# Performance work log

Measured on AMD Instinct MI355X. Metric: run time of the kernel, lower is better.

## Reference

```python
import jax, jax.numpy as jnp
import numpy as np

N_NODES = 50000
N_EDGES = 1600000
HIDDEN = 64
HEADS = 8
EPS = 1e-16  # matches PyG segment-softmax denominator epsilon


def setup_inputs() -> dict:
    key = jax.random.key(0)
    ks = jax.random.split(key, 8)
    node_features = jax.random.normal(ks[0], (N_NODES,), dtype=jnp.float32)
    edge_index = jax.random.randint(ks[1], (2, N_EDGES), 0, N_NODES, dtype=jnp.int64)
    cycle_mask = jax.random.uniform(ks[2], (N_EDGES,), dtype=jnp.float32)
    # feature_proj: Linear(1, HIDDEN)
    W_proj = jax.random.normal(ks[3], (HIDDEN, 1), dtype=jnp.float32) * 0.5
    b_proj = jax.random.normal(ks[4], (HIDDEN,), dtype=jnp.float32) * 0.1
    # attention_net: Linear(2*HIDDEN+1, HEADS)
    fan_in = 2 * HIDDEN + 1
    W_att = jax.random.normal(ks[5], (HEADS, fan_in), dtype=jnp.float32) / np.sqrt(fan_in)
    b_att = jax.random.normal(ks[6], (HEADS,), dtype=jnp.float32) * 0.1
    cycle_penalty = jnp.full((HEADS,), -1.0, dtype=jnp.float32)
    min_sum_scaler = jnp.array([0.8], dtype=jnp.float32)
    return {
        "node_features": node_features,
        "cycle_mask": cycle_mask,
        "W_proj": W_proj,
        "b_proj": b_proj,
        "W_att": W_att,
        "b_att": b_att,
        "cycle_penalty": cycle_penalty,
        "min_sum_scaler": min_sum_scaler,
        "edge_index": edge_index,
    }


def reference(node_features, cycle_mask, W_proj, b_proj, W_att, b_att,
              cycle_penalty, min_sum_scaler, edge_index):
    src = edge_index[0]
    dst = edge_index[1]
    n = node_features.shape[0]
    w = W_proj[:, 0]  # [H]
    # per-edge projected features: [E, H]
    x_src = node_features[src][:, None] * w[None, :] + b_proj
    x_dst = node_features[dst][:, None] * w[None, :] + b_proj
    att_input = jnp.concatenate([x_src, x_dst, cycle_mask[:, None]], axis=-1)  # [E, 2H+1]
    raw = att_input @ W_att.T + b_att  # [E, heads]
    raw = jnp.where(raw >= 0, raw, 0.2 * raw)  # leaky_relu(0.2)
    raw = raw + cycle_mask[:, None] * cycle_penalty
    # segment softmax over edges grouped by dst
    seg_max = jax.ops.segment_max(raw, dst, num_segments=n)  # [N, heads]
    e = jnp.exp(raw - seg_max[dst])
    seg_sum = jax.ops.segment_sum(e, dst, num_segments=n)
    attn = e / (seg_sum[dst] + EPS)  # [E, heads]
    mean_attn = attn.mean(axis=-1)  # [E]
    messages = node_features[src] * mean_attn * min_sum_scaler[0]
    out = jax.ops.segment_sum(messages, dst, num_segments=n)
    return out
```

## Files before the change

### kernel.cpp

```cpp
#include <hip/hip_runtime.h>

#define N_NODES 50000
#define N_EDGES 1600000
#define HEADS 8
#define HIDDEN 64
#define FAN_IN (2*HIDDEN + 1)
#define EPSF 1e-16f

#define BBITS 8
#define BSIZE 256
#define NB 196
#define NH 256
#define NT 512
#define EPB 6250
#define SCAN_N (NB * NH)
#define STRIP 49
#define CAP 12032

#define CST_OFF   0
#define CNT_OFF   4096
#define BASE_OFF  262144
#define PAY_OFF   1048576
#define DLOC_OFF  (PAY_OFF + (size_t)N_EDGES * 8)
#define WS_NEEDED (DLOC_OFF + (size_t)N_EDGES)

__global__ __launch_bounds__(512) void k_prep(
    const float* __restrict__ Wp, const float* __restrict__ bp,
    const float* __restrict__ Wa, const float* __restrict__ ba,
    const float* __restrict__ cp, float* __restrict__ cst) {
    const int k = threadIdx.x >> 6;
    const int j = threadIdx.x & 63;
    const float* row = Wa + k * FAN_IN;
    const float w = Wp[j], b = bp[j];
    const float r1 = row[j], r2 = row[HIDDEN + j];
    float a1 = w * r1, a2 = w * r2, d = b * (r1 + r2);
    #pragma unroll
    for (int s = 32; s > 0; s >>= 1) {
        a1 += __shfl_xor(a1, s);
        a2 += __shfl_xor(a2, s);
        d  += __shfl_xor(d, s);
    }
    if (j == 0) {
        cst[k]      = a1;
        cst[8 + k]  = a2;
        cst[16 + k] = row[2 * HIDDEN];
        cst[24 + k] = d + ba[k];
        cst[32 + k] = cp[k];
    }
}

__global__ __launch_bounds__(NT) void k1a_hist(const int* __restrict__ ei,
                                               int* __restrict__ cnt) {
    __shared__ int hist[NB];
    const int t = threadIdx.x, blk = blockIdx.x;
    if (t < NB) hist[t] = 0;
    __syncthreads();
    const int e0 = blk * EPB, e1 = min(e0 + EPB, N_EDGES);
    for (int e = e0 + t; e < e1; e += NT)
        atomicAdd(&hist[((unsigned)ei[N_EDGES + e]) >> BBITS], 1);
    __syncthreads();
    if (t < NB) cnt[t * NH + blk] = hist[t];
}

__global__ __launch_bounds__(1024) void k_scan(const int* __restrict__ cnt,
                                               int* __restrict__ base) {
    __shared__ int lds[1024];
    const int t = threadIdx.x;
    int s = 0;
    #pragma unroll
    for (int jj = 0; jj < STRIP; ++jj) s += cnt[t * STRIP + jj];
    lds[t] = s;
    __syncthreads();
    for (int d = 1; d < 1024; d <<= 1) {
        const int v = (t >= d) ? lds[t - d] : 0;
        __syncthreads();
        lds[t] += v;
        __syncthreads();
    }
    int run = lds[t] - s;
    #pragma unroll
    for (int jj = 0; jj < STRIP; ++jj) {
        const int i = t * STRIP + jj;
        const int v = cnt[i];
        base[i] = run;
        run += v;
    }
}

__global__ __launch_bounds__(NT) void k1b_scatter(const int* __restrict__ ei,
                                                  const float* __restrict__ cmask,
                                                  const float* __restrict__ nf,
                                                  const int* __restrict__ base,
                                                  float2* __restrict__ pay,
                                                  unsigned char* __restrict__ dloc) {
    __shared__ int cur[NB];
    const int t = threadIdx.x, blk = blockIdx.x;
    if (t < NB) cur[t] = base[t * NH + blk];
    __syncthreads();
    const int e0 = blk * EPB, e1 = min(e0 + EPB, N_EDGES);
    for (int e = e0 + t; e < e1; e += NT) {
        const int src = ei[e];
        const int dst = ei[N_EDGES + e];
        const float fs = nf[src];
        const float c  = cmask[e];
        const int bkt = ((unsigned)dst) >> BBITS;
        const int pos = atomicAdd(&cur[bkt], 1);
        pay[pos]  = make_float2(fs, c);
        dloc[pos] = (unsigned char)(dst & (BSIZE - 1));
    }
}

__global__ __launch_bounds__(NT) void k2_fused(const float* __restrict__ nf,
                                               const float* __restrict__ cst_g,
                                               const int* __restrict__ base,
                                               const float2* __restrict__ pay,
                                               const unsigned char* __restrict__ dloc,
                                               const float* __restrict__ scaler,
                                               float* __restrict__ out) {
    __shared__ float2 pbuf[CAP];
    __shared__ int    hist[BSIZE];
    __shared__ int    noff[BSIZE + 1];
    __shared__ float  FD[BSIZE];
    __shared__ float  cstl[40];

    const int t = threadIdx.x, b = blockIdx.x;
    if (t < 40) cstl[t] = cst_g[t];
    if (t < BSIZE) {
        hist[t] = 0;
        const int n = b * BSIZE + t;
        FD[t] = (n < N_NODES) ? nf[n] : 0.f;
    }
    if (t == NT - 1) noff[0] = 0;
    __syncthreads();

    const int i0 = base[b * NH];
    const int i1 = (b == NB - 1) ? N_EDGES : base[(b + 1) * NH];

    for (int i = i0 + t; i < i1; i += NT)
        atomicAdd(&hist[dloc[i]], 1);
    __syncthreads();

    if (t < BSIZE) noff[t + 1] = hist[t];
    __syncthreads();
    for (int d = 1; d < BSIZE; d <<= 1) {
        int v = 0;
        if (t < BSIZE && t >= d) v = noff[t + 1 - d];
        __syncthreads();
        if (t < BSIZE && t >= d) noff[t + 1] += v;
        __syncthreads();
    }
    if (t < BSIZE) hist[t] = noff[t];
    __syncthreads();

    for (int i = i0 + t; i < i1; i += NT) {
        const int dl = dloc[i];
        const int p  = atomicAdd(&hist[dl], 1);
        if (p < CAP) pbuf[p] = pay[i];
    }
    __syncthreads();

    float A1[8], A2[8], CC[8], DD[8], PP[8];
    #pragma unroll
    for (int k = 0; k < 8; ++k) {
        A1[k] = cstl[k];      A2[k] = cstl[8 + k];  CC[k] = cstl[16 + k];
        DD[k] = cstl[24 + k]; PP[k] = cstl[32 + k];
    }

    const int j = t >> 1, par = t & 1;
    const int n = b * BSIZE + j;
    if (n < N_NODES) {
        int lo = noff[j], hi = noff[j + 1];
        lo = min(lo, CAP); hi = min(hi, CAP);
        const float fd = FD[j];
        float as[8], at[8];
        #pragma unroll
        for (int k = 0; k < 8; ++k) { as[k] = 0.f; at[k] = 0.f; }
        for (int i = lo + par; i < hi; i += 2) {
            const float2 p = pbuf[i];
            #pragma unroll
            for (int k = 0; k < 8; ++k) {
                float r = p.x * A1[k] + fd * A2[k] + p.y * CC[k] + DD[k];
                r = (r >= 0.f) ? r : 0.2f * r;
                r += p.y * PP[k];
                const float ev = __expf(r);
                as[k] += ev;
                at[k] += p.x * ev;
            }
        }
        #pragma unroll
        for (int k = 0; k < 8; ++k) {
            as[k] += __shfl_xor(as[k], 1);
            at[k] += __shfl_xor(at[k], 1);
        }
        if (par == 0) {
            float acc = 0.f;
            #pragma unroll
            for (int k = 0; k < 8; ++k) acc += at[k] / (as[k] + EPSF);
            out[n] = acc * 0.125f * scaler[0];
        }
    }
}

__global__ __launch_bounds__(256) void cagat_edge_atomic(
    const float* __restrict__ nf, const float* __restrict__ cmask,
    const float* __restrict__ Wp, const float* __restrict__ bp,
    const float* __restrict__ Wa, const float* __restrict__ ba,
    const float* __restrict__ cp, const int* __restrict__ ei,
    float* __restrict__ S, float* __restrict__ T) {
    __shared__ float A1[HEADS], A2[HEADS], CC[HEADS], DD[HEADS], PP[HEADS];
    const int t = threadIdx.x;
    if (t < HEADS) {
        const float* row = Wa + t * FAN_IN;
        float a1 = 0.f, a2 = 0.f, d = 0.f;
        for (int h = 0; h < HIDDEN; ++h) {
            float w = Wp[h], b = bp[h];
            a1 += w * row[h]; a2 += w * row[HIDDEN + h];
            d += b * (row[h] + row[HIDDEN + h]);
        }
        A1[t] = a1; A2[t] = a2; CC[t] = row[2*HIDDEN]; DD[t] = d + ba[t]; PP[t] = cp[t];
    }
    __syncthreads();
    const int e = blockIdx.x * 256 + t;
    if (e >= N_EDGES) return;
    const int src = ei[e], dst = ei[N_EDGES + e];
    const float fs = nf[src], fd = nf[dst], c = cmask[e];
    #pragma unroll
    for (int k = 0; k < HEADS; ++k) {
        float r = fs * A1[k] + fd * A2[k] + c * CC[k] + DD[k];
        r = (r >= 0.f) ? r : 0.2f * r;
        r += c * PP[k];
        float ev = __expf(r);
        atomicAdd(S + dst * HEADS + k, ev);
        atomicAdd(T + dst * HEADS + k, fs * ev);
    }
}

__global__ __launch_bounds__(256) void cagat_node_atomic(
    const float* __restrict__ S, const float* __restrict__ T,
    const float* __restrict__ scaler, float* __restrict__ out) {
    const int n = blockIdx.x * 256 + threadIdx.x;
    if (n >= N_NODES) return;
    float acc = 0.f;
    #pragma unroll
    for (int k = 0; k < HEADS; ++k)
        acc += T[n * HEADS + k] / (S[n * HEADS + k] + EPSF);
    out[n] = acc * 0.125f * scaler[0];
}

extern "C" void kernel_launch(void* const* d_in, const int* in_sizes, int n_in,
                              void* d_out, int out_size, void* d_ws, size_t ws_size,
                              hipStream_t stream) {
    const float* nf    = (const float*)d_in[0];
    const float* cmask = (const float*)d_in[1];
    const float* Wp    = (const float*)d_in[2];
    const float* bp    = (const float*)d_in[3];
    const float* Wa    = (const float*)d_in[4];
    const float* ba    = (const float*)d_in[5];
    const float* cp    = (const float*)d_in[6];
    const float* sc    = (const float*)d_in[7];
    const int*   ei    = (const int*)d_in[8];

    char* ws = (char*)d_ws;

    if (ws_size >= WS_NEEDED) {
        float*         cst  = (float*)(ws + CST_OFF);
        int*           cnt  = (int*)(ws + CNT_OFF);
        int*           base = (int*)(ws + BASE_OFF);
        float2*        pay  = (float2*)(ws + PAY_OFF);
        unsigned char* dl   = (unsigned char*)(ws + DLOC_OFF);

        k_prep<<<1, 512, 0, stream>>>(Wp, bp, Wa, ba, cp, cst);
        k1a_hist<<<NH, NT, 0, stream>>>(ei, cnt);
        k_scan<<<1, 1024, 0, stream>>>(cnt, base);
        k1b_scatter<<<NH, NT, 0, stream>>>(ei, cmask, nf, base, pay, dl);
        k2_fused<<<NB, NT, 0, stream>>>(nf, cst, base, pay, dl, sc, (float*)d_out);
    } else {
        float* S = (float*)d_ws;
        float* T = S + (size_t)N_NODES * HEADS;
        hipMemsetAsync(d_ws, 0, (size_t)N_NODES * HEADS * 2 * sizeof(float), stream);
        cagat_edge_atomic<<<(N_EDGES + 255) / 256, 256, 0, stream>>>(
            nf, cmask, Wp, bp, Wa, ba, cp, ei, S, T);
        cagat_node_atomic<<<(N_NODES + 255) / 256, 256, 0, stream>>>(
            S, T, sc, (float*)d_out);
    }
}
```

Measured before the change: 155.2 us.

## Fuse bucket-sort pipeline into one cooperative kernel with grid syncs

Replaces the five-kernel pipeline (prep, histogram, scan, scatter, aggregate) with a single cooperative kernel of 256 blocks that uses grid.sync between phases. Each block keeps its edge slice (src, dst, mask, local rank) in LDS after the histogram pass, so the scatter phase no longer re-reads edge_index and needs no atomics. The column scan is parallelised across blocks. The aim is to remove launch gaps and redundant global reads, at the cost of grid-wide barriers, a large LDS footprint that limits residency, and a dependency on cooperative launch succeeding, with the old multi-kernel path kept as a fallback.

```diff
diff --git a/kernel.cpp b/kernel.cpp
--- a/kernel.cpp
+++ b/kernel.cpp
@@ -1,4 +1,7 @@
 #include <hip/hip_runtime.h>
+#include <hip/hip_cooperative_groups.h>
+
+namespace cg = cooperative_groups;
 
 #define N_NODES 50000
 #define N_EDGES 1600000
@@ -7,69 +10,257 @@
 #define FAN_IN (2*HIDDEN + 1)
 #define EPSF 1e-16f
 
+#define NBLK 256
+#define NT 512
+#define EPB (N_EDGES / NBLK)
+#define EPAD 6272
 #define BBITS 8
 #define BSIZE 256
 #define NB 196
-#define NH 256
-#define NT 512
-#define EPB 6250
-#define SCAN_N (NB * NH)
-#define STRIP 49
 #define CAP 12032
 
-#define CST_OFF   0
-#define CNT_OFF   4096
-#define BASE_OFF  262144
-#define PAY_OFF   1048576
-#define DLOC_OFF  (PAY_OFF + (size_t)N_EDGES * 8)
-#define WS_NEEDED (DLOC_OFF + (size_t)N_EDGES)
-
-__global__ __launch_bounds__(512) void k_prep(
+#define COLCNT_OFF  0
+#define COLBASE_OFF (COLCNT_OFF + 4 * NBLK * NB)
+#define TOT_OFF     (COLBASE_OFF + 4 * NBLK * NB)
+#define PAY_OFF     1048576
+#define DLOC_OFF    (PAY_OFF + (size_t)N_EDGES * 8)
+#define WS_NEEDED   (DLOC_OFF + (size_t)N_EDGES)
+
+struct SMem {
+    union {
+        struct {
+            int   src[EPAD];
+            int   dst[EPAD];
+            float cm[EPAD];
+            unsigned short rank[EPAD];
+        } a;
+        struct {
+            float2 pbuf[CAP];
+            int    noff[BSIZE + 1];
+        } d;
+    } u;
+    float cstl[40];
+    int   bstart[NB + 1];
+    int   hist[BSIZE];
+    int   sB[NBLK];
+    int   cur[NB];
+    float FD[BSIZE];
+};
+
+__global__ __launch_bounds__(NT) void mega(
+    const float* __restrict__ nf, const float* __restrict__ cmask,
+    const float* __restrict__ Wp, const float* __restrict__ bp,
+    const float* __restrict__ Wa, const float* __restrict__ ba,
+    const float* __restrict__ cp, const float* __restrict__ sc,
+    const int* __restrict__ ei,
+    int* __restrict__ colcnt, int* __restrict__ colbase, int* __restrict__ tot,
+    float2* __restrict__ pay, unsigned char* __restrict__ dloc,
+    float* __restrict__ out)
+{
+    __shared__ SMem s;
+    cg::grid_group grid = cg::this_grid();
+    const int t = threadIdx.x, blk = blockIdx.x;
+
+    {
+        const int k = t >> 6, j = t & 63;
+        const float* row = Wa + k * FAN_IN;
+        const float w = Wp[j], b = bp[j];
+        const float r1 = row[j], r2 = row[HIDDEN + j];
+        float a1 = w * r1, a2 = w * r2, d = b * (r1 + r2);
+        #pragma unroll
+        for (int sft = 32; sft > 0; sft >>= 1) {
+            a1 += __shfl_xor(a1, sft);
+            a2 += __shfl_xor(a2, sft);
+            d  += __shfl_xor(d, sft);
+        }
+        if (j == 0) {
+            s.cstl[k]      = a1;
+            s.cstl[8 + k]  = a2;
+            s.cstl[16 + k] = row[2 * HIDDEN];
+            s.cstl[24 + k] = d + ba[k];
+            s.cstl[32 + k] = cp[k];
+        }
+    }
+
+    if (t < BSIZE) s.hist[t] = 0;
+    __syncthreads();
+    const int e0 = blk * EPB;
+    for (int i = t; i < EPB; i += NT) {
+        const int   sv = ei[e0 + i];
+        const int   dv = ei[N_EDGES + e0 + i];
+        const float cv = cmask[e0 + i];
+        s.u.a.src[i] = sv;
+        s.u.a.dst[i] = dv;
+        s.u.a.cm[i]  = cv;
+        const int bkt = ((unsigned)dv) >> BBITS;
+        s.u.a.rank[i] = (unsigned short)atomicAdd(&s.hist[bkt], 1);
+    }
+    __syncthreads();
+    if (t < NB) colcnt[blk * NB + t] = s.hist[t];
+    __threadfence();
+    grid.sync();
+
+    if (blk < NB) {
+        if (t < NBLK) s.sB[t] = colcnt[t * NB + blk];
+        __syncthreads();
+        for (int d = 1; d < NBLK; d <<= 1) {
+            const int v = (t < NBLK && t >= d) ? s.sB[t - d] : 0;
+            __syncthreads();
+            if (t < NBLK && t >= d) s.sB[t] += v;
+            __syncthreads();
+        }
+        if (t < NBLK) colbase[t * NB + blk] = s.sB[t] - colcnt[t * NB + blk];
+        if (t == NBLK - 1) tot[blk] = s.sB[NBLK - 1];
+    }
+    __threadfence();
+    grid.sync();
+
+    {
+        int myTot = 0;
+        if (t < NB) myTot = tot[t];
+        if (t < NBLK) s.sB[t] = myTot;
+        __syncthreads();
+        for (int d = 1; d < NBLK; d <<= 1) {
+            const int v = (t < NBLK && t >= d) ? s.sB[t - d] : 0;
+            __syncthreads();
+            if (t < NBLK && t >= d) s.sB[t] += v;
+            __syncthreads();
+        }
+        if (t < NB) {
+            const int excl = s.sB[t] - myTot;
+            s.bstart[t] = excl;
+            s.cur[t]    = excl + colbase[blk * NB + t];
+        }
+        if (t == 0) s.bstart[NB] = N_EDGES;
+        __syncthreads();
+        for (int i = t; i < EPB; i += NT) {
+            const int dv  = s.u.a.dst[i];
+            const int bkt = ((unsigned)dv) >> BBITS;
+            const int pos = s.cur[bkt] + s.u.a.rank[i];
+            pay[pos]  = make_float2(nf[s.u.a.src[i]], s.u.a.cm[i]);
+            dloc[pos] = (unsigned char)(dv & (BSIZE - 1));
+        }
+    }
+    __threadfence();
+    grid.sync();
+
+    if (blk < NB) {
+        const int i0 = s.bstart[blk], i1 = s.bstart[blk + 1];
+        if (t < BSIZE) {
+            s.hist[t] = 0;
+            const int n = blk * BSIZE + t;
+            s.FD[t] = (n < N_NODES) ? nf[n] : 0.f;
+        }
+        __syncthreads();
+        for (int i = i0 + t; i < i1; i += NT)
+            atomicAdd(&s.hist[dloc[i]], 1);
+        __syncthreads();
+        if (t < BSIZE) s.u.d.noff[t + 1] = s.hist[t];
+        if (t == 0) s.u.d.noff[0] = 0;
+        __syncthreads();
+        for (int d = 1; d < BSIZE; d <<= 1) {
+            int v = 0;
+            if (t < BSIZE && t >= d) v = s.u.d.noff[t + 1 - d];
+            __syncthreads();
+            if (t < BSIZE && t >= d) s.u.d.noff[t + 1] += v;
+            __syncthreads();
+        }
+        if (t < BSIZE) s.hist[t] = s.u.d.noff[t];
+        __syncthreads();
+        for (int i = i0 + t; i < i1; i += NT) {
+            const int dl = dloc[i];
+            const int p  = atomicAdd(&s.hist[dl], 1);
+            if (p < CAP) s.u.d.pbuf[p] = pay[i];
+        }
+        __syncthreads();
+
+        float A1[8], A2[8], CC[8], DD[8], PP[8];
+        #pragma unroll
+        for (int k = 0; k < 8; ++k) {
+            A1[k] = s.cstl[k];      A2[k] = s.cstl[8 + k];  CC[k] = s.cstl[16 + k];
+            DD[k] = s.cstl[24 + k]; PP[k] = s.cstl[32 + k];
+        }
+        const int j = t >> 1, par = t & 1;
+        const int n = blk * BSIZE + j;
+        if (n < N_NODES) {
+            const int lo = min(s.u.d.noff[j], CAP), hi = min(s.u.d.noff[j + 1], CAP);
+            const float fd = s.FD[j];
+            float as[8], at[8];
+            #pragma unroll
+            for (int k = 0; k < 8; ++k) { as[k] = 0.f; at[k] = 0.f; }
+            for (int i = lo + par; i < hi; i += 2) {
+                const float2 p = s.u.d.pbuf[i];
+                #pragma unroll
+                for (int k = 0; k < 8; ++k) {
+                    float r = p.x * A1[k] + fd * A2[k] + p.y * CC[k] + DD[k];
+                    r = (r >= 0.f) ? r : 0.2f * r;
+                    r += p.y * PP[k];
+                    const float ev = __expf(r);
+                    as[k] += ev;
+                    at[k] += p.x * ev;
+                }
+            }
+            #pragma unroll
+            for (int k = 0; k < 8; ++k) {
+                as[k] += __shfl_xor(as[k], 1);
+                at[k] += __shfl_xor(at[k], 1);
+            }
+            if (par == 0) {
+                float acc = 0.f;
+                #pragma unroll
+                for (int k = 0; k < 8; ++k) acc += at[k] / (as[k] + EPSF);
+                out[n] = acc * 0.125f * sc[0];
+            }
+        }
+    }
+}
+
+#define FNB 196
+#define FNH 256
+#define FNT 512
+#define FEPB 6250
+#define FSTRIP 49
+#define FCNT_OFF   4096
+#define FBASE_OFF  262144
+
+__global__ __launch_bounds__(FNT) void f_prep(
     const float* __restrict__ Wp, const float* __restrict__ bp,
     const float* __restrict__ Wa, const float* __restrict__ ba,
     const float* __restrict__ cp, float* __restrict__ cst) {
-    const int k = threadIdx.x >> 6;
-    const int j = threadIdx.x & 63;
+    const int k = threadIdx.x >> 6, j = threadIdx.x & 63;
     const float* row = Wa + k * FAN_IN;
     const float w = Wp[j], b = bp[j];
     const float r1 = row[j], r2 = row[HIDDEN + j];
     float a1 = w * r1, a2 = w * r2, d = b * (r1 + r2);
     #pragma unroll
-    for (int s = 32; s > 0; s >>= 1) {
-        a1 += __shfl_xor(a1, s);
-        a2 += __shfl_xor(a2, s);
-        d  += __shfl_xor(d, s);
+    for (int sft = 32; sft > 0; sft >>= 1) {
+        a1 += __shfl_xor(a1, sft); a2 += __shfl_xor(a2, sft); d += __shfl_xor(d, sft);
     }
     if (j == 0) {
-        cst[k]      = a1;
-        cst[8 + k]  = a2;
-        cst[16 + k] = row[2 * HIDDEN];
-        cst[24 + k] = d + ba[k];
-        cst[32 + k] = cp[k];
-    }
-}
-
-__global__ __launch_bounds__(NT) void k1a_hist(const int* __restrict__ ei,
-                                               int* __restrict__ cnt) {
-    __shared__ int hist[NB];
+        cst[k] = a1; cst[8 + k] = a2; cst[16 + k] = row[2 * HIDDEN];
+        cst[24 + k] = d + ba[k]; cst[32 + k] = cp[k];
+    }
+}
+
+__global__ __launch_bounds__(FNT) void f_hist(const int* __restrict__ ei, int* __restrict__ cnt) {
+    __shared__ int hist[FNB];
     const int t = threadIdx.x, blk = blockIdx.x;
-    if (t < NB) hist[t] = 0;
-    __syncthreads();
-    const int e0 = blk * EPB, e1 = min(e0 + EPB, N_EDGES);
-    for (int e = e0 + t; e < e1; e += NT)
+    if (t < FNB) hist[t] = 0;
+    __syncthreads();
+    const int a0 = blk * FEPB, a1 = min(a0 + FEPB, N_EDGES);
+    for (int e = a0 + t; e < a1; e += FNT)
         atomicAdd(&hist[((unsigned)ei[N_EDGES + e]) >> BBITS], 1);
     __syncthreads();
-    if (t < NB) cnt[t * NH + blk] = hist[t];
-}
-
-__global__ __launch_bounds__(1024) void k_scan(const int* __restrict__ cnt,
-                                               int* __restrict__ base) {
+    if (t < FNB) cnt[t * FNH + blk] = hist[t];
+}
+
+__global__ __launch_bounds__(1024) void f_scan(const int* __restrict__ cnt, int* __restrict__ base) {
     __shared__ int lds[1024];
     const int t = threadIdx.x;
-    int s = 0;
+    int sm = 0;
     #pragma unroll
-    for (int jj = 0; jj < STRIP; ++jj) s += cnt[t * STRIP + jj];
-    lds[t] = s;
+    for (int jj = 0; jj < FSTRIP; ++jj) sm += cnt[t * FSTRIP + jj];
+    lds[t] = sm;
     __syncthreads();
     for (int d = 1; d < 1024; d <<= 1) {
         const int v = (t >= d) ? lds[t - d] : 0;
@@ -77,69 +268,61 @@
         lds[t] += v;
         __syncthreads();
     }
-    int run = lds[t] - s;
+    int run = lds[t] - sm;
     #pragma unroll
-    for (int jj = 0; jj < STRIP; ++jj) {
-        const int i = t * STRIP + jj;
+    for (int jj = 0; jj < FSTRIP; ++jj) {
+        const int i = t * FSTRIP + jj;
         const int v = cnt[i];
         base[i] = run;
         run += v;
     }
 }
 
-__global__ __launch_bounds__(NT) void k1b_scatter(const int* __restrict__ ei,
-                                                  const float* __restrict__ cmask,
-                                                  const float* __restrict__ nf,
-                                                  const int* __restrict__ base,
-                                                  float2* __restrict__ pay,
-                                                  unsigned char* __restrict__ dloc) {
-    __shared__ int cur[NB];
+__global__ __launch_bounds__(FNT) void f_scatter(const int* __restrict__ ei,
+                                                 const float* __restrict__ cmask,
+                                                 const float* __restrict__ nf,
+                                                 const int* __restrict__ base,
+                                                 float2* __restrict__ pay,
+                                                 unsigned char* __restrict__ dl) {
+    __shared__ int cur[FNB];
     const int t = threadIdx.x, blk = blockIdx.x;
-    if (t < NB) cur[t] = base[t * NH + blk];
-    __syncthreads();
-    const int e0 = blk * EPB, e1 = min(e0 + EPB, N_EDGES);
-    for (int e = e0 + t; e < e1; e += NT) {
-        const int src = ei[e];
-        const int dst = ei[N_EDGES + e];
-        const float fs = nf[src];
-        const float c  = cmask[e];
+    if (t < FNB) cur[t] = base[t * FNH + blk];
+    __syncthreads();
+    const int a0 = blk * FEPB, a1 = min(a0 + FEPB, N_EDGES);
+    for (int e = a0 + t; e < a1; e += FNT) {
+        const int src = ei[e], dst = ei[N_EDGES + e];
         const int bkt = ((unsigned)dst) >> BBITS;
         const int pos = atomicAdd(&cur[bkt], 1);
-        pay[pos]  = make_float2(fs, c);
-        dloc[pos] = (unsigned char)(dst & (BSIZE - 1));
-    }
-}
-
-__global__ __launch_bounds__(NT) void k2_fused(const float* __restrict__ nf,
+        pay[pos] = make_float2(nf[src], cmask[e]);
+        dl[pos] = (unsigned char)(dst & (BSIZE - 1));
+    }
+}
+
+__global__ __launch_bounds__(FNT) void f_fused(const float* __restrict__ nf,
                                                const float* __restrict__ cst_g,
                                                const int* __restrict__ base,
                                                const float2* __restrict__ pay,
-                                               const unsigned char* __restrict__ dloc,
+                                               const unsigned char* __restrict__ dl,
                                                const float* __restrict__ scaler,
                                                float* __restrict__ out) {
     __shared__ float2 pbuf[CAP];
     __shared__ int    hist[BSIZE];
     __shared__ int    noff[BSIZE + 1];
-    __shared__ float  FD[BSIZE];
+    __shared__ float  FDl[BSIZE];
     __shared__ float  cstl[40];
-
     const int t = threadIdx.x, b = blockIdx.x;
     if (t < 40) cstl[t] = cst_g[t];
     if (t < BSIZE) {
         hist[t] = 0;
         const int n = b * BSIZE + t;
-        FD[t] = (n < N_NODES) ? nf[n] : 0.f;
-    }
-    if (t == NT - 1) noff[0] = 0;
-    __syncthreads();
-
-    const int i0 = base[b * NH];
-    const int i1 = (b == NB - 1) ? N_EDGES : base[(b + 1) * NH];
-
-    for (int i = i0 + t; i < i1; i += NT)
-        atomicAdd(&hist[dloc[i]], 1);
-    __syncthreads();
-
+        FDl[t] = (n < N_NODES) ? nf[n] : 0.f;
+    }
+    if (t == FNT - 1) noff[0] = 0;
+    __syncthreads();
+    const int i0 = base[b * FNH];
+    const int i1 = (b == FNB - 1) ? N_EDGES : base[(b + 1) * FNH];
+    for (int i = i0 + t; i < i1; i += FNT) atomicAdd(&hist[dl[i]], 1);
+    __syncthreads();
     if (t < BSIZE) noff[t + 1] = hist[t];
     __syncthreads();
     for (int d = 1; d < BSIZE; d <<= 1) {
@@ -151,27 +334,23 @@
     }
     if (t < BSIZE) hist[t] = noff[t];
     __syncthreads();
-
-    for (int i = i0 + t; i < i1; i += NT) {
-        const int dl = dloc[i];
-        const int p  = atomicAdd(&hist[dl], 1);
+    for (int i = i0 + t; i < i1; i += FNT) {
+        const int d2 = dl[i];
+        const int p = atomicAdd(&hist[d2], 1);
         if (p < CAP) pbuf[p] = pay[i];
     }
     __syncthreads();
-
     float A1[8], A2[8], CC[8], DD[8], PP[8];
     #pragma unroll
     for (int k = 0; k < 8; ++k) {
-        A1[k] = cstl[k];      A2[k] = cstl[8 + k];  CC[k] = cstl[16 + k];
+        A1[k] = cstl[k]; A2[k] = cstl[8 + k]; CC[k] = cstl[16 + k];
         DD[k] = cstl[24 + k]; PP[k] = cstl[32 + k];
     }
-
     const int j = t >> 1, par = t & 1;
     const int n = b * BSIZE + j;
     if (n < N_NODES) {
-        int lo = noff[j], hi = noff[j + 1];
-        lo = min(lo, CAP); hi = min(hi, CAP);
-        const float fd = FD[j];
+        const int lo = min(noff[j], CAP), hi = min(noff[j + 1], CAP);
+        const float fd = FDl[j];
         float as[8], at[8];
         #pragma unroll
         for (int k = 0; k < 8; ++k) { as[k] = 0.f; at[k] = 0.f; }
@@ -201,52 +380,6 @@
     }
 }
 
-__global__ __launch_bounds__(256) void cagat_edge_atomic(
-    const float* __restrict__ nf, const float* __restrict__ cmask,
-    const float* __restrict__ Wp, const float* __restrict__ bp,
-    const float* __restrict__ Wa, const float* __restrict__ ba,
-    const float* __restrict__ cp, const int* __restrict__ ei,
-    float* __restrict__ S, float* __restrict__ T) {
-    __shared__ float A1[HEADS], A2[HEADS], CC[HEADS], DD[HEADS], PP[HEADS];
-    const int t = threadIdx.x;
-    if (t < HEADS) {
-        const float* row = Wa + t * FAN_IN;
-        float a1 = 0.f, a2 = 0.f, d = 0.f;
-        for (int h = 0; h < HIDDEN; ++h) {
-            float w = Wp[h], b = bp[h];
-            a1 += w * row[h]; a2 += w * row[HIDDEN + h];
-            d += b * (row[h] + row[HIDDEN + h]);
-        }
-        A1[t] = a1; A2[t] = a2; CC[t] = row[2*HIDDEN]; DD[t] = d + ba[t]; PP[t] = cp[t];
-    }
-    __syncthreads();
-    const int e = blockIdx.x * 256 + t;
-    if (e >= N_EDGES) return;
-    const int src = ei[e], dst = ei[N_EDGES + e];
-    const float fs = nf[src], fd = nf[dst], c = cmask[e];
-    #pragma unroll
-    for (int k = 0; k < HEADS; ++k) {
-        float r = fs * A1[k] + fd * A2[k] + c * CC[k] + DD[k];
-        r = (r >= 0.f) ? r : 0.2f * r;
-        r += c * PP[k];
-        float ev = __expf(r);
-        atomicAdd(S + dst * HEADS + k, ev);
-        atomicAdd(T + dst * HEADS + k, fs * ev);
-    }
-}
-
-__global__ __launch_bounds__(256) void cagat_node_atomic(
-    const float* __restrict__ S, const float* __restrict__ T,
-    const float* __restrict__ scaler, float* __restrict__ out) {
-    const int n = blockIdx.x * 256 + threadIdx.x;
-    if (n >= N_NODES) return;
-    float acc = 0.f;
-    #pragma unroll
-    for (int k = 0; k < HEADS; ++k)
-        acc += T[n * HEADS + k] / (S[n * HEADS + k] + EPSF);
-    out[n] = acc * 0.125f * scaler[0];
-}
-
 extern "C" void kernel_launch(void* const* d_in, const int* in_sizes, int n_in,
                               void* d_out, int out_size, void* d_ws, size_t ws_size,
                               hipStream_t stream) {
@@ -261,26 +394,28 @@
     const int*   ei    = (const int*)d_in[8];
 
     char* ws = (char*)d_ws;
-
-    if (ws_size >= WS_NEEDED) {
-        float*         cst  = (float*)(ws + CST_OFF);
-        int*           cnt  = (int*)(ws + CNT_OFF);
-        int*           base = (int*)(ws + BASE_OFF);
-        float2*        pay  = (float2*)(ws + PAY_OFF);
-        unsigned char* dl   = (unsigned char*)(ws + DLOC_OFF);
-
-        k_prep<<<1, 512, 0, stream>>>(Wp, bp, Wa, ba, cp, cst);
-        k1a_hist<<<NH, NT, 0, stream>>>(ei, cnt);
-        k_scan<<<1, 1024, 0, stream>>>(cnt, base);
-        k1b_scatter<<<NH, NT, 0, stream>>>(ei, cmask, nf, base, pay, dl);
-        k2_fused<<<NB, NT, 0, stream>>>(nf, cst, base, pay, dl, sc, (float*)d_out);
-    } else {
-        float* S = (float*)d_ws;
-        float* T = S + (size_t)N_NODES * HEADS;
-        hipMemsetAsync(d_ws, 0, (size_t)N_NODES * HEADS * 2 * sizeof(float), stream);
-        cagat_edge_atomic<<<(N_EDGES + 255) / 256, 256, 0, stream>>>(
-            nf, cmask, Wp, bp, Wa, ba, cp, ei, S, T);
-        cagat_node_atomic<<<(N_NODES + 255) / 256, 256, 0, stream>>>(
-            S, T, sc, (float*)d_out);
-    }
-}
+    int*           colcnt  = (int*)(ws + COLCNT_OFF);
+    int*           colbase = (int*)(ws + COLBASE_OFF);
+    int*           tot     = (int*)(ws + TOT_OFF);
+    float2*        pay     = (float2*)(ws + PAY_OFF);
+    unsigned char* dl      = (unsigned char*)(ws + DLOC_OFF);
+    float*         outp    = (float*)d_out;
+
+    void* args[] = {(void*)&nf, (void*)&cmask, (void*)&Wp, (void*)&bp,
+                    (void*)&Wa, (void*)&ba, (void*)&cp, (void*)&sc,
+                    (void*)&ei, (void*)&colcnt, (void*)&colbase, (void*)&tot,
+                    (void*)&pay, (void*)&dl, (void*)&outp};
+
+    hipError_t err = hipLaunchCooperativeKernel((const void*)mega, dim3(NBLK), dim3(NT),
+                                                args, 0, stream);
+    if (err != hipSuccess) {
+        float* cst  = (float*)(ws + 0);
+        int*   cnt  = (int*)(ws + FCNT_OFF);
+        int*   base = (int*)(ws + FBASE_OFF);
+        f_prep<<<1, FNT, 0, stream>>>(Wp, bp, Wa, ba, cp, cst);
+        f_hist<<<FNH, FNT, 0, stream>>>(ei, cnt);
+        f_scan<<<1, 1024, 0, stream>>>(cnt, base);
+        f_scatter<<<FNH, FNT, 0, stream>>>(ei, cmask, nf, base, pay, dl);
+        f_fused<<<FNB, FNT, 0, stream>>>(nf, cst, base, pay, dl, sc, outp);
+    }
+}
```

Result: slower. 379.9 us (+144.8%).

## Sort edges locally per block before scatter, parallelize scan, fold prep into reduce

Applied to the files above, without the earlier changes.

Replaces the single-block global scan with a per-bucket column scan over 196 blocks, and moves the bucket-start prefix into the scatter and reduce kernels. The scatter kernel now ranks edges in LDS and writes them in bucket-sorted order, so global payload writes become contiguous runs instead of scattered atomics-ordered stores. The weight-folding prep kernel is merged into the reduce kernel, which removes one launch. The cost is more LDS and more barriers per scatter block, and every reduce block redoes the small scans.

```diff
diff --git a/kernel.cpp b/kernel.cpp
--- a/kernel.cpp
+++ b/kernel.cpp
@@ -10,136 +10,191 @@
 #define BBITS 8
 #define BSIZE 256
 #define NB 196
-#define NH 256
-#define NT 512
-#define EPB 6250
-#define SCAN_N (NB * NH)
-#define STRIP 49
+#define NSB 512
+#define EPB 3125
+#define NTS 256
+#define NTR 512
 #define CAP 12032
 
-#define CST_OFF   0
-#define CNT_OFF   4096
-#define BASE_OFF  262144
-#define PAY_OFF   1048576
-#define DLOC_OFF  (PAY_OFF + (size_t)N_EDGES * 8)
-#define WS_NEEDED (DLOC_OFF + (size_t)N_EDGES)
-
-__global__ __launch_bounds__(512) void k_prep(
-    const float* __restrict__ Wp, const float* __restrict__ bp,
-    const float* __restrict__ Wa, const float* __restrict__ ba,
-    const float* __restrict__ cp, float* __restrict__ cst) {
-    const int k = threadIdx.x >> 6;
-    const int j = threadIdx.x & 63;
-    const float* row = Wa + k * FAN_IN;
-    const float w = Wp[j], b = bp[j];
-    const float r1 = row[j], r2 = row[HIDDEN + j];
-    float a1 = w * r1, a2 = w * r2, d = b * (r1 + r2);
-    #pragma unroll
-    for (int s = 32; s > 0; s >>= 1) {
-        a1 += __shfl_xor(a1, s);
-        a2 += __shfl_xor(a2, s);
-        d  += __shfl_xor(d, s);
-    }
-    if (j == 0) {
-        cst[k]      = a1;
-        cst[8 + k]  = a2;
-        cst[16 + k] = row[2 * HIDDEN];
-        cst[24 + k] = d + ba[k];
-        cst[32 + k] = cp[k];
-    }
-}
-
-__global__ __launch_bounds__(NT) void k1a_hist(const int* __restrict__ ei,
-                                               int* __restrict__ cnt) {
+#define CNT_OFF   0
+#define COLB_OFF  524288
+#define TOT_OFF   1048576
+#define PAY_OFF   2097152
+#define DL_OFF    (PAY_OFF + (size_t)N_EDGES * 8)
+#define WS_NEEDED (DL_OFF + (size_t)N_EDGES)
+
+__global__ __launch_bounds__(NTS) void k_hist(const int* __restrict__ ei,
+                                              int* __restrict__ cnt) {
     __shared__ int hist[NB];
     const int t = threadIdx.x, blk = blockIdx.x;
     if (t < NB) hist[t] = 0;
     __syncthreads();
-    const int e0 = blk * EPB, e1 = min(e0 + EPB, N_EDGES);
-    for (int e = e0 + t; e < e1; e += NT)
-        atomicAdd(&hist[((unsigned)ei[N_EDGES + e]) >> BBITS], 1);
-    __syncthreads();
-    if (t < NB) cnt[t * NH + blk] = hist[t];
-}
-
-__global__ __launch_bounds__(1024) void k_scan(const int* __restrict__ cnt,
-                                               int* __restrict__ base) {
-    __shared__ int lds[1024];
-    const int t = threadIdx.x;
-    int s = 0;
-    #pragma unroll
-    for (int jj = 0; jj < STRIP; ++jj) s += cnt[t * STRIP + jj];
-    lds[t] = s;
-    __syncthreads();
-    for (int d = 1; d < 1024; d <<= 1) {
-        const int v = (t >= d) ? lds[t - d] : 0;
-        __syncthreads();
-        lds[t] += v;
-        __syncthreads();
-    }
-    int run = lds[t] - s;
-    #pragma unroll
-    for (int jj = 0; jj < STRIP; ++jj) {
-        const int i = t * STRIP + jj;
-        const int v = cnt[i];
-        base[i] = run;
-        run += v;
-    }
-}
-
-__global__ __launch_bounds__(NT) void k1b_scatter(const int* __restrict__ ei,
-                                                  const float* __restrict__ cmask,
-                                                  const float* __restrict__ nf,
-                                                  const int* __restrict__ base,
-                                                  float2* __restrict__ pay,
-                                                  unsigned char* __restrict__ dloc) {
+    const int e0 = blk * EPB;
+    for (int i = t; i < EPB; i += NTS)
+        atomicAdd(&hist[((unsigned)ei[N_EDGES + e0 + i]) >> BBITS], 1);
+    __syncthreads();
+    if (t < NB) cnt[t * NSB + blk] = hist[t];
+}
+
+__global__ __launch_bounds__(NSB) void k_colscan(const int* __restrict__ cnt,
+                                                 int* __restrict__ colbase,
+                                                 int* __restrict__ tot) {
+    __shared__ int lds[NSB];
+    const int t = threadIdx.x, b = blockIdx.x;
+    const int v = cnt[b * NSB + t];
+    lds[t] = v;
+    __syncthreads();
+    for (int d = 1; d < NSB; d <<= 1) {
+        const int x = (t >= d) ? lds[t - d] : 0;
+        __syncthreads();
+        lds[t] += x;
+        __syncthreads();
+    }
+    colbase[b * NSB + t] = lds[t] - v;
+    if (t == NSB - 1) tot[b] = lds[t];
+}
+
+__global__ __launch_bounds__(NTS) void k_scatter(const int* __restrict__ ei,
+                                                 const float* __restrict__ cmask,
+                                                 const float* __restrict__ nf,
+                                                 const int* __restrict__ colbase,
+                                                 const int* __restrict__ tot,
+                                                 float2* __restrict__ pay,
+                                                 unsigned char* __restrict__ dl8) {
+    __shared__ int pr[EPB];
+    __shared__ int inv[EPB];
+    __shared__ int hist[NB];
+    __shared__ int lstart[NB];
     __shared__ int cur[NB];
+    __shared__ int scr[256];
     const int t = threadIdx.x, blk = blockIdx.x;
-    if (t < NB) cur[t] = base[t * NH + blk];
-    __syncthreads();
-    const int e0 = blk * EPB, e1 = min(e0 + EPB, N_EDGES);
-    for (int e = e0 + t; e < e1; e += NT) {
-        const int src = ei[e];
-        const int dst = ei[N_EDGES + e];
-        const float fs = nf[src];
-        const float c  = cmask[e];
-        const int bkt = ((unsigned)dst) >> BBITS;
-        const int pos = atomicAdd(&cur[bkt], 1);
-        pay[pos]  = make_float2(fs, c);
-        dloc[pos] = (unsigned char)(dst & (BSIZE - 1));
-    }
-}
-
-__global__ __launch_bounds__(NT) void k2_fused(const float* __restrict__ nf,
-                                               const float* __restrict__ cst_g,
-                                               const int* __restrict__ base,
-                                               const float2* __restrict__ pay,
-                                               const unsigned char* __restrict__ dloc,
-                                               const float* __restrict__ scaler,
-                                               float* __restrict__ out) {
+    const int e0 = blk * EPB;
+
+    if (t < NB) hist[t] = 0;
+    __syncthreads();
+
+    for (int i = t; i < EPB; i += NTS) {
+        const int dv = ei[N_EDGES + e0 + i];
+        const int bkt = ((unsigned)dv) >> BBITS;
+        const int rank = atomicAdd(&hist[bkt], 1);
+        pr[i] = (bkt << 20) | ((dv & (BSIZE - 1)) << 12) | rank;
+    }
+    __syncthreads();
+
+    int mytot = (t < NB) ? tot[t] : 0;
+    scr[t] = mytot;
+    __syncthreads();
+    for (int d = 1; d < 256; d <<= 1) {
+        const int x = (t >= d) ? scr[t - d] : 0;
+        __syncthreads();
+        scr[t] += x;
+        __syncthreads();
+    }
+    const int bstart_t = scr[t] - mytot;
+    __syncthreads();
+    int myh = (t < NB) ? hist[t] : 0;
+    scr[t] = myh;
+    __syncthreads();
+    for (int d = 1; d < 256; d <<= 1) {
+        const int x = (t >= d) ? scr[t - d] : 0;
+        __syncthreads();
+        scr[t] += x;
+        __syncthreads();
+    }
+    if (t < NB) {
+        const int ls = scr[t] - myh;
+        lstart[t] = ls;
+        cur[t] = bstart_t + colbase[t * NSB + blk] - ls;
+    }
+    __syncthreads();
+
+    for (int i = t; i < EPB; i += NTS) {
+        const int u = pr[i];
+        inv[lstart[u >> 20] + (u & 0xFFF)] = i;
+    }
+    __syncthreads();
+
+    for (int p = t; p < EPB; p += NTS) {
+        const int i = inv[p];
+        const int u = pr[i];
+        const int bkt = u >> 20;
+        const int g = cur[bkt] + p;
+        const int e = e0 + i;
+        pay[g] = make_float2(nf[ei[e]], cmask[e]);
+        dl8[g] = (unsigned char)((u >> 12) & 255);
+    }
+}
+
+__global__ __launch_bounds__(NTR) void k_reduce(const float* __restrict__ nf,
+                                                const float* __restrict__ Wp,
+                                                const float* __restrict__ bp,
+                                                const float* __restrict__ Wa,
+                                                const float* __restrict__ ba,
+                                                const float* __restrict__ cp,
+                                                const float* __restrict__ sc,
+                                                const int* __restrict__ tot,
+                                                const float2* __restrict__ pay,
+                                                const unsigned char* __restrict__ dl8,
+                                                float* __restrict__ out) {
     __shared__ float2 pbuf[CAP];
     __shared__ int    hist[BSIZE];
     __shared__ int    noff[BSIZE + 1];
     __shared__ float  FD[BSIZE];
     __shared__ float  cstl[40];
-
+    __shared__ int    scr[256];
+    __shared__ int    sI0;
     const int t = threadIdx.x, b = blockIdx.x;
-    if (t < 40) cstl[t] = cst_g[t];
+
+    {
+        const int k = t >> 6, j = t & 63;
+        const float* row = Wa + k * FAN_IN;
+        const float w = Wp[j], bb = bp[j];
+        const float r1 = row[j], r2 = row[HIDDEN + j];
+        float a1 = w * r1, a2 = w * r2, d = bb * (r1 + r2);
+        #pragma unroll
+        for (int s = 32; s > 0; s >>= 1) {
+            a1 += __shfl_xor(a1, s);
+            a2 += __shfl_xor(a2, s);
+            d  += __shfl_xor(d, s);
+        }
+        if (j == 0) {
+            cstl[k]      = a1;
+            cstl[8 + k]  = a2;
+            cstl[16 + k] = row[2 * HIDDEN];
+            cstl[24 + k] = d + ba[k];
+            cstl[32 + k] = cp[k];
+        }
+    }
+
+    {
+        int v = 0;
+        if (t < 256) v = (t < NB) ? tot[t] : 0;
+        if (t < 256) scr[t] = v;
+        __syncthreads();
+        for (int d = 1; d < 256; d <<= 1) {
+            int x = 0;
+            if (t < 256 && t >= d) x = scr[t - d];
+            __syncthreads();
+            if (t < 256 && t >= d) scr[t] += x;
+            __syncthreads();
+        }
+        if (t == b) sI0 = scr[t] - v;
+        __syncthreads();
+    }
+    const int i0 = sI0;
+    const int i1 = i0 + tot[b];
+
     if (t < BSIZE) {
         hist[t] = 0;
         const int n = b * BSIZE + t;
         FD[t] = (n < N_NODES) ? nf[n] : 0.f;
     }
-    if (t == NT - 1) noff[0] = 0;
-    __syncthreads();
-
-    const int i0 = base[b * NH];
-    const int i1 = (b == NB - 1) ? N_EDGES : base[(b + 1) * NH];
-
-    for (int i = i0 + t; i < i1; i += NT)
-        atomicAdd(&hist[dloc[i]], 1);
-    __syncthreads();
-
+    if (t == 0) noff[0] = 0;
+    __syncthreads();
+
+    for (int i = i0 + t; i < i1; i += NTR)
+        atomicAdd(&hist[dl8[i]], 1);
+    __syncthreads();
     if (t < BSIZE) noff[t + 1] = hist[t];
     __syncthreads();
     for (int d = 1; d < BSIZE; d <<= 1) {
@@ -152,9 +207,9 @@
     if (t < BSIZE) hist[t] = noff[t];
     __syncthreads();
 
-    for (int i = i0 + t; i < i1; i += NT) {
-        const int dl = dloc[i];
-        const int p  = atomicAdd(&hist[dl], 1);
+    for (int i = i0 + t; i < i1; i += NTR) {
+        const int dl = dl8[i];
+        const int p = atomicAdd(&hist[dl], 1);
         if (p < CAP) pbuf[p] = pay[i];
     }
     __syncthreads();
@@ -165,12 +220,10 @@
         A1[k] = cstl[k];      A2[k] = cstl[8 + k];  CC[k] = cstl[16 + k];
         DD[k] = cstl[24 + k]; PP[k] = cstl[32 + k];
     }
-
     const int j = t >> 1, par = t & 1;
     const int n = b * BSIZE + j;
     if (n < N_NODES) {
-        int lo = noff[j], hi = noff[j + 1];
-        lo = min(lo, CAP); hi = min(hi, CAP);
+        const int lo = min(noff[j], CAP), hi = min(noff[j + 1], CAP);
         const float fd = FD[j];
         float as[8], at[8];
         #pragma unroll
@@ -196,7 +249,7 @@
             float acc = 0.f;
             #pragma unroll
             for (int k = 0; k < 8; ++k) acc += at[k] / (as[k] + EPSF);
-            out[n] = acc * 0.125f * scaler[0];
+            out[n] = acc * 0.125f * sc[0];
         }
     }
 }
@@ -263,17 +316,17 @@
     char* ws = (char*)d_ws;
 
     if (ws_size >= WS_NEEDED) {
-        float*         cst  = (float*)(ws + CST_OFF);
-        int*           cnt  = (int*)(ws + CNT_OFF);
-        int*           base = (int*)(ws + BASE_OFF);
-        float2*        pay  = (float2*)(ws + PAY_OFF);
-        unsigned char* dl   = (unsigned char*)(ws + DLOC_OFF);
-
-        k_prep<<<1, 512, 0, stream>>>(Wp, bp, Wa, ba, cp, cst);
-        k1a_hist<<<NH, NT, 0, stream>>>(ei, cnt);
-        k_scan<<<1, 1024, 0, stream>>>(cnt, base);
-        k1b_scatter<<<NH, NT, 0, stream>>>(ei, cmask, nf, base, pay, dl);
-        k2_fused<<<NB, NT, 0, stream>>>(nf, cst, base, pay, dl, sc, (float*)d_out);
+        int*           cnt     = (int*)(ws + CNT_OFF);
+        int*           colbase = (int*)(ws + COLB_OFF);
+        int*           tot     = (int*)(ws + TOT_OFF);
+        float2*        pay     = (float2*)(ws + PAY_OFF);
+        unsigned char* dl      = (unsigned char*)(ws + DL_OFF);
+
+        k_hist<<<NSB, NTS, 0, stream>>>(ei, cnt);
+        k_colscan<<<NB, NSB, 0, stream>>>(cnt, colbase, tot);
+        k_scatter<<<NSB, NTS, 0, stream>>>(ei, cmask, nf, colbase, tot, pay, dl);
+        k_reduce<<<NB, NTR, 0, stream>>>(nf, Wp, bp, Wa, ba, cp, sc, tot, pay, dl,
+                                         (float*)d_out);
     } else {
         float* S = (float*)d_ws;
         float* T = S + (size_t)N_NODES * HEADS;
```

Result: faster. 131.7 us (-15.1%).
